# Kernel optimization log

Measured on AMD Instinct MI355X. Metric: run time of the kernel, lower is better.

Reference implementation:

```python
import jax, jax.numpy as jnp
import numpy as np

NUM_HEADS = 8
HEAD_SPLITS = [2, 3, 3]   # heads per conv window group (windows 3,5,7)


def _dwconv(x, w, b):
    # depthwise conv2d, SAME padding; x [B,Cg,H,W], w [Cg,1,k,k]
    k = w.shape[-1]
    pad = k // 2
    out = jax.lax.conv_general_dilated(
        x, w, window_strides=(1, 1), padding=[(pad, pad), (pad, pad)],
        feature_group_count=x.shape[1])
    return out + b[None, :, None, None]


def setup_inputs() -> dict:
    key = jax.random.key(0)
    ks = jax.random.split(key, 8)
    B, Hs, Ws, C = 16, 56, 56, 512
    N = 1 + Hs * Ws
    Ch = C // NUM_HEADS
    inp = {
        "x": jax.random.normal(ks[0], (B, N, C), dtype=jnp.float32),
        "qkv_w": jax.random.normal(ks[1], (3 * C, C), dtype=jnp.float32) * 0.02,
        "qkv_b": jnp.zeros((3 * C,), dtype=jnp.float32),
        "proj_w": jax.random.normal(ks[2], (C, C), dtype=jnp.float32) * 0.02,
        "proj_b": jnp.zeros((C,), dtype=jnp.float32),
        "conv_w3": jax.random.normal(ks[3], (2 * Ch, 1, 3, 3), dtype=jnp.float32) * 0.1,
        "conv_b3": jnp.zeros((2 * Ch,), dtype=jnp.float32),
        "conv_w5": jax.random.normal(ks[4], (3 * Ch, 1, 5, 5), dtype=jnp.float32) * 0.1,
        "conv_b5": jnp.zeros((3 * Ch,), dtype=jnp.float32),
        "conv_w7": jax.random.normal(ks[5], (3 * Ch, 1, 7, 7), dtype=jnp.float32) * 0.1,
        "conv_b7": jnp.zeros((3 * Ch,), dtype=jnp.float32),
        "H": 56,
        "W": 56,
    }
    return inp


def reference(x, qkv_w, qkv_b, proj_w, proj_b,
              conv_w3, conv_b3, conv_w5, conv_b5, conv_w7, conv_b7, H, W):
    B, N, C = x.shape
    h = NUM_HEADS
    Ch = C // h
    scale = Ch ** -0.5

    # qkv projection -> [3, B, h, N, Ch]
    qkv = (x @ qkv_w.T + qkv_b).reshape(B, N, 3, h, Ch)
    qkv = jnp.transpose(qkv, (2, 0, 3, 1, 4))
    q, k, v = qkv[0], qkv[1], qkv[2]

    # linear-attention factorization: softmax over tokens, then small Ch x Ch matmuls
    k_sm = jax.nn.softmax(k, axis=2)                     # softmax over N
    kv = jnp.einsum('bhnk,bhnd->bhkd', k_sm, v)          # [B,h,Ch,Ch]
    factor_att = jnp.einsum('bhnk,bhkd->bhnd', q, kv)    # [B,h,N,Ch]

    # conv relative-position encoding (CoaT ConvRelPosEnc)
    q_img = q[:, :, 1:, :]                               # drop CLS token
    v_img = v[:, :, 1:, :]
    v_img = jnp.transpose(v_img, (0, 1, 3, 2)).reshape(B, h * Ch, H, W)
    splits = np.cumsum([s * Ch for s in HEAD_SPLITS])[:-1]
    p3, p5, p7 = jnp.split(v_img, splits, axis=1)
    conv_v = jnp.concatenate([
        _dwconv(p3, conv_w3, conv_b3),
        _dwconv(p5, conv_w5, conv_b5),
        _dwconv(p7, conv_w7, conv_b7)], axis=1)           # [B,h*Ch,H,W]
    conv_v = jnp.transpose(conv_v.reshape(B, h, Ch, H * W), (0, 1, 3, 2))
    ev = q_img * conv_v                                   # [B,h,HW,Ch]
    crpe = jnp.concatenate(
        [jnp.zeros((B, h, 1, Ch), dtype=x.dtype), ev], axis=2)

    out = scale * factor_att + crpe                       # [B,h,N,Ch]
    out = jnp.transpose(out, (0, 2, 1, 3)).reshape(B, N, C)
    return out @ proj_w.T + proj_b
```

## Files before the change

kernel.cpp:

```cpp
#include <hip/hip_runtime.h>
#include <stdint.h>

#define NHEADS 8
#define NTOK   3137
#define BATCH  16
#define CDIM   512
#define MT     (BATCH*NTOK)

typedef unsigned short u16;
typedef float f32x4  __attribute__((ext_vector_type(4)));
typedef short bf16x8 __attribute__((ext_vector_type(8)));

__device__ __forceinline__ float bf2f(u16 u){
  union { uint32_t i; float f; } x; x.i = ((uint32_t)u) << 16; return x.f;
}
__device__ __forceinline__ u16 f2bf(float f){
  union { float f; uint32_t i; } x; x.f = f;
  uint32_t r = x.i + 0x7fffu + ((x.i >> 16) & 1u);
  return (u16)(r >> 16);
}
__device__ __forceinline__ void async_ld16(void* lds, const void* g){
  __builtin_amdgcn_global_load_lds((const __attribute__((address_space(1))) void*)g,
                                   (__attribute__((address_space(3))) void*)lds, 16, 0, 0);
}
#define MFMA16(d,a,b) d = __builtin_amdgcn_mfma_f32_16x16x32_bf16(a,b,d,0,0,0)

__global__ void cvt_kernel(const float* __restrict__ src, u16* __restrict__ dst, int n4){
  int i = blockIdx.x * blockDim.x + threadIdx.x;
  if (i < n4){
    float4 v = ((const float4*)src)[i];
    uint32_t lo = ((uint32_t)f2bf(v.y) << 16) | f2bf(v.x);
    uint32_t hi = ((uint32_t)f2bf(v.w) << 16) | f2bf(v.z);
    ((uint2*)dst)[i] = make_uint2(lo, hi);
  }
}

template<int MODE>
__global__ __launch_bounds__(512, 2) void gemm2(
    const u16* __restrict__ A, const u16* __restrict__ Bw, const float* __restrict__ bias,
    u16* __restrict__ q_s, u16* __restrict__ k_s, u16* __restrict__ v_s,
    float* __restrict__ outF, int M)
{
  constexpr int BM=256, BN=256, WN=4;
  constexpr int THREADS = 512;
  constexpr int MF = 8, NF = 4;
  constexpr int WROWS = 128, WCOLS = 64;
  __shared__ __align__(16) u16 smem[2*(BM+BN)*64];

  const int t = threadIdx.x;
  const int w = t >> 6, l = t & 63;
  const int wr = w / WN, wc = w % WN;
  const int lr = l & 15, lg = l >> 4;

  const int nx = gridDim.x;
  const int nwg = nx * gridDim.y;
  const int orig = blockIdx.y * nx + blockIdx.x;
  const int q8 = nwg >> 3, r8 = nwg & 7;
  const int xcd = orig & 7;
  const int wgid = (xcd < r8 ? xcd*(q8+1) : r8*(q8+1) + (xcd-r8)*q8) + (orig >> 3);
  const int n0 = (wgid % nx) * BN;
  const int m0 = (wgid / nx) * BM;

  f32x4 acc[MF][NF];
#pragma unroll
  for (int i=0;i<MF;i++)
#pragma unroll
    for (int j=0;j<NF;j++) acc[i][j] = (f32x4){0.f,0.f,0.f,0.f};

  auto stage = [&](int bi, int k0){
    u16* da = smem + bi*(BM*64);
    u16* db = smem + 2*BM*64 + bi*(BN*64);
#pragma unroll
    for (int j=0;j<(BM*8)/THREADS;j++){
      int qc = t + THREADS*j;
      int R = qc >> 3, c = qc & 7;
      int cs = (c ^ (R & 7)) * 8;
      int ar = m0 + R; if (ar > M-1) ar = M-1;
      async_ld16(&da[qc*8], &A[(size_t)ar*512 + k0 + cs]);
    }
#pragma unroll
    for (int j=0;j<(BN*8)/THREADS;j++){
      int qc = t + THREADS*j;
      int R = qc >> 3, c = qc & 7;
      int cs = (c ^ (R & 7)) * 8;
      async_ld16(&db[qc*8], &Bw[(size_t)(n0+R)*512 + k0 + cs]);
    }
  };

  stage(0, 0);
  __syncthreads();
  int cur = 0;
  for (int kt = 0; kt < 8; ++kt){
    if (kt < 7) stage(cur ^ 1, (kt+1)*64);
    const u16* a_base = smem + cur*(BM*64);
    const u16* b_base = smem + 2*BM*64 + cur*(BN*64);
    __builtin_amdgcn_s_setprio(1);
#pragma unroll
    for (int ks=0; ks<2; ks++){
      bf16x8 af[MF], bfv[NF];
      int chunk = ks*4 + lg;
#pragma unroll
      for (int fi=0;fi<MF;fi++){
        int row = wr*WROWS + fi*16 + lr;
        af[fi] = *(const bf16x8*)&a_base[row*64 + ((chunk ^ (row & 7))*8)];
      }
#pragma unroll
      for (int fj=0;fj<NF;fj++){
        int col = wc*WCOLS + fj*16 + lr;
        bfv[fj] = *(const bf16x8*)&b_base[col*64 + ((chunk ^ (col & 7))*8)];
      }
#pragma unroll
      for (int fi=0;fi<MF;fi++)
#pragma unroll
        for (int fj=0;fj<NF;fj++)
          acc[fi][fj] = __builtin_amdgcn_mfma_f32_16x16x32_bf16(af[fi], bfv[fj], acc[fi][fj], 0, 0, 0);
    }
    __builtin_amdgcn_s_setprio(0);
    __syncthreads();
    cur ^= 1;
  }

  float bvv[NF];
#pragma unroll
  for (int fj=0;fj<NF;fj++) bvv[fj] = bias[n0 + wc*WCOLS + fj*16 + lr];

  if (MODE == 0){
    u16* warea = smem + w * (WROWS*WCOLS);
#pragma unroll
    for (int fi=0;fi<MF;fi++)
#pragma unroll
      for (int fj=0;fj<NF;fj++)
#pragma unroll
        for (int r=0;r<4;r++)
          warea[(fi*16 + lg*4 + r)*WCOLS + fj*16 + lr] = f2bf(acc[fi][fj][r] + bvv[fj]);
    __syncthreads();
    const int colo = n0 + wc*WCOLS;
    const int part = colo >> 9;
    const int hq   = (colo >> 6) & 7;
    u16* dst = (part == 0) ? q_s : ((part == 1) ? k_s : v_s);
    const int rsub = l >> 3;
    const int csub = (l & 7) * 8;
#pragma unroll
    for (int pass=0; pass<WROWS/8; ++pass){
      int rl = pass*8 + rsub;
      int m = m0 + wr*WROWS + rl;
      if (m < M){
        int bb = m / NTOK;
        int n  = m - bb*NTOK;
        uint4 vv = *(const uint4*)&warea[rl*WCOLS + csub];
        *(uint4*)&dst[((size_t)(bb*8 + hq)*NTOK + n)*64 + csub] = vv;
      }
    }
  } else {
    constexpr int PR = WROWS/2;
    float* warea = (float*)smem + w * (PR*WCOLS);
    const int colo = n0 + wc*WCOLS;
    const int rsub = l >> 4;
    const int csub = (l & 15) * 4;
#pragma unroll
    for (int p=0; p<2; ++p){
#pragma unroll
      for (int fh=0; fh<MF/2; fh++){
        int fi = p*(MF/2) + fh;
#pragma unroll
        for (int fj=0;fj<NF;fj++)
#pragma unroll
          for (int r=0;r<4;r++)
            warea[(fh*16 + lg*4 + r)*WCOLS + fj*16 + lr] = acc[fi][fj][r] + bvv[fj];
      }
#pragma unroll
      for (int pass=0; pass<PR/4; ++pass){
        int rl = pass*4 + rsub;
        int m = m0 + wr*WROWS + p*PR + rl;
        if (m < M){
          float4 vv = *(const float4*)&warea[rl*WCOLS + csub];
          *(float4*)&outF[(size_t)m*512 + colo + csub] = vv;
        }
      }
    }
  }
}

__global__ __launch_bounds__(256) void kv_mfma(
    const u16* __restrict__ k_s, const u16* __restrict__ v_s,
    float* __restrict__ kv_p, float* __restrict__ s_p)
{
  __shared__ __align__(16) u16 ekT[64*64];
  __shared__ __align__(16) u16 vT[64*64];
  __shared__ float part_s[32*64];
  const int t  = threadIdx.x;
  const int bh = blockIdx.x;
  const int qq = blockIdx.y;
  const size_t base = (size_t)bh * NTOK * 64;
  const int c_beg = (qq==0) ? 0 : (qq==1) ? 13 : (qq==2) ? 26 : 39;
  const int c_end = (qq==3) ? 50 : (c_beg + 13);
  const int w = t >> 6, l = t & 63;
  const int lr = l & 15, lg = l >> 4;
  const int nl0 = t >> 3;
  const int dc  = (t & 7) * 8;

  f32x4 acc[4];
#pragma unroll
  for (int j=0;j<4;j++) acc[j] = (f32x4){0.f,0.f,0.f,0.f};
  float s_loc[8];
#pragma unroll
  for (int i=0;i<8;i++) s_loc[i] = 0.f;

  for (int ch = c_beg; ch < c_end; ++ch){
    const int n0c = ch*64;
    __syncthreads();
#pragma unroll
    for (int half=0; half<2; ++half){
      int nloc = nl0 + half*32;
      int n = n0c + nloc;
      bool valid = (n < NTOK);
      uint4 kvec = make_uint4(0u,0u,0u,0u), vvec = make_uint4(0u,0u,0u,0u);
      if (valid){
        kvec = *(const uint4*)&k_s[base + (size_t)n*64 + dc];
        vvec = *(const uint4*)&v_s[base + (size_t)n*64 + dc];
      }
      const u16* kp = (const u16*)&kvec;
      const u16* vp = (const u16*)&vvec;
      const int nc = nloc >> 3, ne = nloc & 7;
#pragma unroll
      for (int i=0;i<8;i++){
        float e = valid ? __expf(bf2f(kp[i])) : 0.f;
        s_loc[i] += e;
        int row = dc + i;
        int pos = row*64 + ((nc ^ (row & 7) ^ ((row >> 3) & 7))*8) + ne;
        ekT[pos] = f2bf(e);
        vT[pos]  = valid ? vp[i] : (u16)0;
      }
    }
    __syncthreads();
    __builtin_amdgcn_s_setprio(1);
#pragma unroll
    for (int ks=0; ks<2; ks++){
      int chnk = ks*4 + lg;
      int arow = w*16 + lr;
      bf16x8 af = *(const bf16x8*)&ekT[arow*64 + ((chnk ^ (arow & 7) ^ ((arow >> 3) & 7))*8)];
#pragma unroll
      for (int fj=0; fj<4; fj++){
        int col = fj*16 + lr;
        bf16x8 bv = *(const bf16x8*)&vT[col*64 + ((chnk ^ (col & 7) ^ ((col >> 3) & 7))*8)];
        MFMA16(acc[fj], af, bv);
      }
    }
    __builtin_amdgcn_s_setprio(0);
  }

  const size_t obase = ((size_t)qq*128 + bh) * 4096;
#pragma unroll
  for (int fj=0; fj<4; fj++)
#pragma unroll
    for (int r=0; r<4; r++)
      kv_p[obase + (size_t)(w*16 + lg*4 + r)*64 + fj*16 + lr] = acc[fj][r];

#pragma unroll
  for (int i=0;i<8;i++) part_s[nl0*64 + dc + i] = s_loc[i];
  __syncthreads();
  if (t < 64){
    float s = 0.f;
    for (int r=0;r<32;r++) s += part_s[r*64 + t];
    s_p[((size_t)qq*128 + bh)*64 + t] = s;
  }
}

__global__ void kv_reduce(const float* __restrict__ kv_p, const float* __restrict__ s_p,
                          u16* __restrict__ kvT){
  const int bh = blockIdx.x, t = threadIdx.x;
  for (int i=0;i<16;i++){
    int e = t*16 + i;
    int k = e >> 6, d = e & 63;
    float v = 0.f, S = 0.f;
#pragma unroll
    for (int hf=0; hf<4; hf++){
      v += kv_p[(size_t)(hf*128 + bh)*4096 + e];
      S += s_p[(hf*128 + bh)*64 + k];
    }
    kvT[(size_t)bh*4096 + d*64 + k] = f2bf(v / S);
  }
}

template<int R>
__global__ __launch_bounds__(256) void conv_fa(
    const u16* __restrict__ v_s, const u16* __restrict__ q_s,
    const u16* __restrict__ kvT,
    const float* __restrict__ wsrc, const float* __restrict__ bsrc,
    int h0, u16* __restrict__ out_pre)
{
  constexpr int KK = 2*R + 1;
  constexpr int TAPS = KK*KK;
  __shared__ __align__(16) u16 smem[8192 + KK*3584];
  u16* vt = smem + 8192;
  const int t = threadIdx.x;
  const int y  = blockIdx.x;
  const int hh = blockIdx.y;
  const int b  = blockIdx.z;
  const int h  = h0 + hh;
  const int bh = b*8 + h;
  const size_t base = (size_t)bh * NTOK * 64;
  const int n0 = 1 + y*56;

#pragma unroll
  for (int j=0;j<2;j++){
    int qq = t + 256*j;
    int row = qq >> 3, c = qq & 7;
    int cs = (c ^ (row & 7)) * 8;
    int n = n0 + row; if (n > NTOK-1) n = NTOK-1;
    async_ld16(&smem[qq*8], &q_s[base + (size_t)n*64 + cs]);
    async_ld16(&smem[4096 + qq*8], &kvT[(size_t)bh*4096 + row*64 + cs]);
  }
  for (int ry=0; ry<KK; ry++){
    int yy = y - R + ry;
    for (int idx = t; idx < 448; idx += 256){
      uint4 val = make_uint4(0u,0u,0u,0u);
      if (yy >= 0 && yy < 56)
        val = *(const uint4*)&v_s[base + (size_t)(1 + yy*56)*64 + idx*8];
      *(uint4*)&vt[ry*3584 + idx*8] = val;
    }
  }
  __syncthreads();

  const int w = t >> 6, l = t & 63;
  const int lr = l & 15, lg = l >> 4;
  f32x4 fac[4];
#pragma unroll
  for (int j=0;j<4;j++) fac[j] = (f32x4){0.f,0.f,0.f,0.f};
#pragma unroll
  for (int ks=0; ks<2; ks++){
    int chunk = ks*4 + lg;
    int arow = w*16 + lr;
    bf16x8 af = *(const bf16x8*)&smem[arow*64 + ((chunk ^ (arow & 7))*8)];
#pragma unroll
    for (int fj=0; fj<4; fj++){
      int col = fj*16 + lr;
      bf16x8 bvv = *(const bf16x8*)&smem[4096 + col*64 + ((chunk ^ (col & 7))*8)];
      MFMA16(fac[fj], af, bvv);
    }
  }

  const int d = l;
  const int xg = w;
  float wreg[TAPS];
#pragma unroll
  for (int i=0;i<TAPS;i++) wreg[i] = wsrc[(hh*64 + d)*TAPS + i];
  const float bias = bsrc[hh*64 + d];
  float creg[14];
#pragma unroll
  for (int i=0;i<14;i++) creg[i] = bias;
  const int x0 = xg * 14;
#pragma unroll
  for (int ry=0; ry<KK; ry++){
    float rw[14 + 2*R];
#pragma unroll
    for (int i=0; i<14+2*R; i++){
      int xx = x0 - R + i;
      rw[i] = (xx >= 0 && xx < 56) ? bf2f(vt[ry*3584 + xx*64 + d]) : 0.f;
    }
#pragma unroll
    for (int xi=0; xi<14; xi++)
#pragma unroll
      for (int rx=0; rx<KK; rx++)
        creg[xi] += rw[xi+rx] * wreg[ry*KK + rx];
  }

  float qv[14];
#pragma unroll
  for (int xi=0; xi<14; xi++){
    int row = x0 + xi;
    int chunk = d >> 3, e = d & 7;
    qv[xi] = bf2f(smem[row*64 + ((chunk ^ (row & 7))*8) + e]);
  }

  __syncthreads();
  float* fa = (float*)smem;
#pragma unroll
  for (int fj=0; fj<4; fj++)
#pragma unroll
    for (int r=0; r<4; r++)
      fa[(w*16 + lg*4 + r)*64 + fj*16 + lr] = 0.125f * fac[fj][r];
  __syncthreads();

#pragma unroll
  for (int xi=0; xi<14; xi++){
    int nn = n0 + x0 + xi;
    out_pre[((size_t)b*NTOK + nn)*CDIM + h*64 + d] =
        f2bf(fa[(x0 + xi)*64 + d] + creg[xi]*qv[xi]);
  }
}

__global__ void fa0_kernel(const u16* __restrict__ q_s, const u16* __restrict__ kvT,
                           u16* __restrict__ out_pre){
  const int b = blockIdx.x, t = threadIdx.x;
  const int h = t >> 6, d = t & 63;
  const int bh = b*8 + h;
  float s = 0.f;
#pragma unroll
  for (int k=0; k<64; k++)
    s += bf2f(q_s[(size_t)bh*NTOK*64 + k]) * bf2f(kvT[(size_t)bh*4096 + d*64 + k]);
  out_pre[(size_t)b*NTOK*CDIM + h*64 + d] = f2bf(0.125f * s);
}

extern "C" void kernel_launch(void* const* d_in, const int* in_sizes, int n_in,
                              void* d_out, int out_size, void* d_ws, size_t ws_size,
                              hipStream_t stream)
{
  const float* x      = (const float*)d_in[0];
  const float* qkv_w  = (const float*)d_in[1];
  const float* qkv_b  = (const float*)d_in[2];
  const float* proj_w = (const float*)d_in[3];
  const float* proj_b = (const float*)d_in[4];
  const float* w3 = (const float*)d_in[5];
  const float* b3 = (const float*)d_in[6];
  const float* w5 = (const float*)d_in[7];
  const float* b5 = (const float*)d_in[8];
  const float* w7 = (const float*)d_in[9];
  const float* b7 = (const float*)d_in[10];
  float* out = (float*)d_out;

  char* ws = (char*)d_ws;
  size_t off = 0;
  auto alloc = [&](size_t bytes) -> void* {
    void* p = ws + off;
    off += (bytes + 255) & ~(size_t)255;
    return p;
  };
  u16*   x_bf     = (u16*)alloc((size_t)MT*512*2);
  u16*   qkvw_bf  = (u16*)alloc((size_t)1536*512*2);
  u16*   projw_bf = (u16*)alloc((size_t)512*512*2);
  u16*   q_s      = (u16*)alloc((size_t)128*NTOK*64*2);
  u16*   k_s      = (u16*)alloc((size_t)128*NTOK*64*2);
  u16*   v_s      = (u16*)alloc((size_t)128*NTOK*64*2);
  u16*   kvT      = (u16*)alloc((size_t)128*4096*2);
  float* kv_p     = (float*)alloc((size_t)4*128*4096*4);
  float* s_p      = (float*)alloc((size_t)4*128*64*4);
  u16*   out_pre  = x_bf;

  { int n4 = (MT*512)/4;   cvt_kernel<<<(n4+255)/256, 256, 0, stream>>>(x, x_bf, n4); }
  { int n4 = (1536*512)/4; cvt_kernel<<<(n4+255)/256, 256, 0, stream>>>(qkv_w, qkvw_bf, n4); }
  { int n4 = (512*512)/4;  cvt_kernel<<<(n4+255)/256, 256, 0, stream>>>(proj_w, projw_bf, n4); }

  gemm2<0><<<dim3(6, 197), 512, 0, stream>>>(x_bf, qkvw_bf, qkv_b, q_s, k_s, v_s, nullptr, MT);

  kv_mfma<<<dim3(128, 4), 256, 0, stream>>>(k_s, v_s, kv_p, s_p);
  kv_reduce<<<128, 256, 0, stream>>>(kv_p, s_p, kvT);
  fa0_kernel<<<16, 512, 0, stream>>>(q_s, kvT, out_pre);

  conv_fa<1><<<dim3(56, 2, 16), 256, 0, stream>>>(v_s, q_s, kvT, w3, b3, 0, out_pre);
  conv_fa<2><<<dim3(56, 3, 16), 256, 0, stream>>>(v_s, q_s, kvT, w5, b5, 2, out_pre);
  conv_fa<3><<<dim3(56, 3, 16), 256, 0, stream>>>(v_s, q_s, kvT, w7, b7, 5, out_pre);

  gemm2<1><<<dim3(2, 197), 512, 0, stream>>>(out_pre, projw_bf, proj_b, nullptr, nullptr, nullptr, out, MT);
}
```

Measured before the change: 351.7 us.

## Split kv accumulation eight ways, prefetch next chunk, fuse CLS-token output into reduce

The kv_mfma kernel now splits the 50 token chunks across 8 blocks per head instead of 4, which doubles the grid for more parallelism. It also software-prefetches the next chunk's k/v vectors into registers before the barrier, so global load latency overlaps with the LDS fill and MFMA work. kv_reduce is reorganised to sum 8 partials and to compute the CLS-token factor attention (q0 · kv) itself, which removes the separate fa0 kernel launch. The cost is more partial buffers to reduce, higher register pressure from the prefetch registers, and a little extra shared memory in the reduce kernel.

```diff
diff --git a/kernel.cpp b/kernel.cpp
--- a/kernel.cpp
+++ b/kernel.cpp
@@ -192,8 +192,8 @@
   const int bh = blockIdx.x;
   const int qq = blockIdx.y;
   const size_t base = (size_t)bh * NTOK * 64;
-  const int c_beg = (qq==0) ? 0 : (qq==1) ? 13 : (qq==2) ? 26 : 39;
-  const int c_end = (qq==3) ? 50 : (c_beg + 13);
+  const int c_beg = qq*6 + (qq < 2 ? qq : 2);
+  const int c_end = c_beg + 6 + (qq < 2 ? 1 : 0);
   const int w = t >> 6, l = t & 63;
   const int lr = l & 15, lg = l >> 4;
   const int nl0 = t >> 3;
@@ -206,19 +206,31 @@
 #pragma unroll
   for (int i=0;i<8;i++) s_loc[i] = 0.f;
 
+  auto LD = [&](int ch, int half, uint4& kv, uint4& vv){
+    int n = ch*64 + nl0 + half*32;
+    if (n < NTOK){
+      kv = *(const uint4*)&k_s[base + (size_t)n*64 + dc];
+      vv = *(const uint4*)&v_s[base + (size_t)n*64 + dc];
+    } else {
+      kv = make_uint4(0u,0u,0u,0u);
+      vv = make_uint4(0u,0u,0u,0u);
+    }
+  };
+
+  uint4 kc0, vc0, kc1, vc1, kn0, vn0, kn1, vn1;
+  LD(c_beg, 0, kc0, vc0);
+  LD(c_beg, 1, kc1, vc1);
+
   for (int ch = c_beg; ch < c_end; ++ch){
     const int n0c = ch*64;
+    if (ch + 1 < c_end){ LD(ch+1, 0, kn0, vn0); LD(ch+1, 1, kn1, vn1); }
     __syncthreads();
 #pragma unroll
     for (int half=0; half<2; ++half){
+      const uint4& kvec = half ? kc1 : kc0;
+      const uint4& vvec = half ? vc1 : vc0;
       int nloc = nl0 + half*32;
-      int n = n0c + nloc;
-      bool valid = (n < NTOK);
-      uint4 kvec = make_uint4(0u,0u,0u,0u), vvec = make_uint4(0u,0u,0u,0u);
-      if (valid){
-        kvec = *(const uint4*)&k_s[base + (size_t)n*64 + dc];
-        vvec = *(const uint4*)&v_s[base + (size_t)n*64 + dc];
-      }
+      bool valid = (n0c + nloc < NTOK);
       const u16* kp = (const u16*)&kvec;
       const u16* vp = (const u16*)&vvec;
       const int nc = nloc >> 3, ne = nloc & 7;
@@ -229,7 +241,7 @@
         int row = dc + i;
         int pos = row*64 + ((nc ^ (row & 7) ^ ((row >> 3) & 7))*8) + ne;
         ekT[pos] = f2bf(e);
-        vT[pos]  = valid ? vp[i] : (u16)0;
+        vT[pos]  = vp[i];
       }
     }
     __syncthreads();
@@ -247,6 +259,7 @@
       }
     }
     __builtin_amdgcn_s_setprio(0);
+    kc0 = kn0; vc0 = vn0; kc1 = kn1; vc1 = vn1;
   }
 
   const size_t obase = ((size_t)qq*128 + bh) * 4096;
@@ -267,18 +280,32 @@
 }
 
 __global__ void kv_reduce(const float* __restrict__ kv_p, const float* __restrict__ s_p,
-                          u16* __restrict__ kvT){
+                          const u16* __restrict__ q_s, u16* __restrict__ kvT,
+                          u16* __restrict__ out_pre){
+  __shared__ float red[64*64];
   const int bh = blockIdx.x, t = threadIdx.x;
+  const int b = bh >> 3, h = bh & 7;
+  const int k = t >> 2;
+  const float q0 = bf2f(q_s[(size_t)bh*NTOK*64 + k]);
+  float S = 0.f;
+#pragma unroll
+  for (int hf=0; hf<8; hf++) S += s_p[(hf*128 + bh)*64 + k];
+  const float rS = 1.f / S;
   for (int i=0;i<16;i++){
     int e = t*16 + i;
-    int k = e >> 6, d = e & 63;
-    float v = 0.f, S = 0.f;
-#pragma unroll
-    for (int hf=0; hf<4; hf++){
-      v += kv_p[(size_t)(hf*128 + bh)*4096 + e];
-      S += s_p[(hf*128 + bh)*64 + k];
-    }
-    kvT[(size_t)bh*4096 + d*64 + k] = f2bf(v / S);
+    int d = (t & 3)*16 + i;
+    float v = 0.f;
+#pragma unroll
+    for (int hf=0; hf<8; hf++) v += kv_p[(size_t)(hf*128 + bh)*4096 + e];
+    float val = v * rS;
+    kvT[(size_t)bh*4096 + d*64 + k] = f2bf(val);
+    red[k*64 + d] = val * q0;
+  }
+  __syncthreads();
+  if (t < 64){
+    float s = 0.f;
+    for (int r=0;r<64;r++) s += red[r*64 + t];
+    out_pre[((size_t)b*NTOK)*CDIM + h*64 + t] = f2bf(0.125f * s);
   }
 }
 
@@ -390,18 +417,6 @@
   }
 }
 
-__global__ void fa0_kernel(const u16* __restrict__ q_s, const u16* __restrict__ kvT,
-                           u16* __restrict__ out_pre){
-  const int b = blockIdx.x, t = threadIdx.x;
-  const int h = t >> 6, d = t & 63;
-  const int bh = b*8 + h;
-  float s = 0.f;
-#pragma unroll
-  for (int k=0; k<64; k++)
-    s += bf2f(q_s[(size_t)bh*NTOK*64 + k]) * bf2f(kvT[(size_t)bh*4096 + d*64 + k]);
-  out_pre[(size_t)b*NTOK*CDIM + h*64 + d] = f2bf(0.125f * s);
-}
-
 extern "C" void kernel_launch(void* const* d_in, const int* in_sizes, int n_in,
                               void* d_out, int out_size, void* d_ws, size_t ws_size,
                               hipStream_t stream)
@@ -433,8 +448,8 @@
   u16*   k_s      = (u16*)alloc((size_t)128*NTOK*64*2);
   u16*   v_s      = (u16*)alloc((size_t)128*NTOK*64*2);
   u16*   kvT      = (u16*)alloc((size_t)128*4096*2);
-  float* kv_p     = (float*)alloc((size_t)4*128*4096*4);
-  float* s_p      = (float*)alloc((size_t)4*128*64*4);
+  float* kv_p     = (float*)alloc((size_t)8*128*4096*4);
+  float* s_p      = (float*)alloc((size_t)8*128*64*4);
   u16*   out_pre  = x_bf;
 
   { int n4 = (MT*512)/4;   cvt_kernel<<<(n4+255)/256, 256, 0, stream>>>(x, x_bf, n4); }
@@ -443,9 +458,8 @@
 
   gemm2<0><<<dim3(6, 197), 512, 0, stream>>>(x_bf, qkvw_bf, qkv_b, q_s, k_s, v_s, nullptr, MT);
 
-  kv_mfma<<<dim3(128, 4), 256, 0, stream>>>(k_s, v_s, kv_p, s_p);
-  kv_reduce<<<128, 256, 0, stream>>>(kv_p, s_p, kvT);
-  fa0_kernel<<<16, 512, 0, stream>>>(q_s, kvT, out_pre);
+  kv_mfma<<<dim3(128, 8), 256, 0, stream>>>(k_s, v_s, kv_p, s_p);
+  kv_reduce<<<128, 256, 0, stream>>>(kv_p, s_p, q_s, kvT, out_pre);
 
   conv_fa<1><<<dim3(56, 2, 16), 256, 0, stream>>>(v_s, q_s, kvT, w3, b3, 0, out_pre);
   conv_fa<2><<<dim3(56, 3, 16), 256, 0, stream>>>(v_s, q_s, kvT, w5, b5, 2, out_pre);
```

Result: no change. 345.9 us (-1.6%).
